# Performance work log

Hardware: AMD Instinct MI355X
Metric: run time of the kernel (lower is better)

Reference implementation:

```python
import jax, jax.numpy as jnp
import numpy as np

B, T, C, H = 4, 2048, 1024, 16
D = C // H

def setup_inputs() -> dict:
    key = jax.random.key(0)
    k1, k2, k3, k4 = jax.random.split(key, 4)
    s = 1.0 / np.sqrt(C)
    return {
        "x": jax.random.normal(k1, (B, T, C), dtype=jnp.float32),
        "W_qkv": jax.random.normal(k2, (3 * C, C), dtype=jnp.float32) * s,
        "W_out": jax.random.normal(k3, (C, C), dtype=jnp.float32) * s,
        "b_out": jax.random.normal(k4, (C,), dtype=jnp.float32) * s,
    }

def reference(x, W_qkv, W_out, b_out):
    Bx, Tx, Cx = x.shape
    # qkv projection (torch Linear: y = x @ W.T), bias=False
    qkv = x @ W_qkv.T                               # [B,T,3C]
    q, k, v = jnp.split(qkv, 3, axis=-1)
    def heads(t):
        return t.reshape(Bx, Tx, H, D).transpose(0, 2, 1, 3)  # [B,H,T,D]
    q, k, v = heads(q), heads(k), heads(v)
    scale = 1.0 / jnp.sqrt(jnp.asarray(D, dtype=x.dtype))
    scores = jnp.einsum("bhqd,bhkd->bhqk", q, k) * scale      # [B,H,T,T]
    causal = jnp.tril(jnp.ones((Tx, Tx), dtype=bool))
    scores = jnp.where(causal[None, None], scores, -jnp.inf)
    attn = jax.nn.softmax(scores, axis=-1)                    # dropout p=0 (eval)
    out = jnp.einsum("bhqk,bhkd->bhqd", attn, v)              # [B,H,T,D]
    out = out.transpose(0, 2, 1, 3).reshape(Bx, Tx, Cx)       # [B,T,C]
    return out @ W_out.T + b_out
```

## Files before the change

### kernel.cpp

```cpp
#include <hip/hip_runtime.h>


typedef __attribute__((ext_vector_type(8))) __bf16 bf16x8;
typedef __attribute__((ext_vector_type(4))) float f32x4;
typedef __attribute__((ext_vector_type(16))) float f32x16;

__device__ __forceinline__ unsigned short f2bf(float f) {
  union { float f; unsigned u; } v; v.f = f;
  unsigned r = v.u + 0x7fffu + ((v.u >> 16) & 1u);
  return (unsigned short)(r >> 16);
}

__device__ __forceinline__ unsigned cvtpk(float lo, float hi) {
  unsigned r;
  asm("v_cvt_pk_bf16_f32 %0, %1, %2" : "=v"(r) : "v"(lo), "v"(hi));
  return r;
}

__device__ __forceinline__ void gld16(const void* g, void* l) {
  __builtin_amdgcn_global_load_lds(
      (const __attribute__((address_space(1))) void*)g,
      (__attribute__((address_space(3))) void*)l, 16, 0, 0);
}

__device__ __forceinline__ f32x4 mfma16(bf16x8 a, bf16x8 b, f32x4 c) {
  return __builtin_amdgcn_mfma_f32_16x16x32_bf16(a, b, c, 0, 0, 0);
}
__device__ __forceinline__ f32x16 mfma32(bf16x8 a, bf16x8 b, f32x16 c) {
  return __builtin_amdgcn_mfma_f32_32x32x16_bf16(a, b, c, 0, 0, 0);
}

__global__ __launch_bounds__(256) void cast_f32_bf16(
    const float* __restrict__ src, unsigned short* __restrict__ dst, int n) {
  int i = (blockIdx.x * 256 + threadIdx.x) * 4;
  if (i >= n) return;
  float4 v = *(const float4*)(src + i);
  ushort4 o;
  o.x = f2bf(v.x); o.y = f2bf(v.y); o.z = f2bf(v.z); o.w = f2bf(v.w);
  *(ushort4*)(dst + i) = o;
}

__device__ __forceinline__ bf16x8 ldsw128(const char* mat, int row, int cb) {
  return *(const bf16x8*)(mat + row * 128 + (cb ^ ((row & 7) << 4)));
}


#define PH_SYNC_A() do { __builtin_amdgcn_s_barrier();              \
    asm volatile("s_waitcnt lgkmcnt(0)" ::: "memory");              \
    __builtin_amdgcn_sched_barrier(0); } while (0)
#define PH_SYNC_B() do { __builtin_amdgcn_s_barrier();              \
    __builtin_amdgcn_sched_barrier(0); } while (0)
#define VMC6() asm volatile("s_waitcnt vmcnt(6)" ::: "memory")
#define VMC0() asm volatile("s_waitcnt vmcnt(0)" ::: "memory")

#define QUAD(MH, NH, AF, BF) do {                                   \
    __builtin_amdgcn_s_setprio(1);                                  \
    _Pragma("unroll") for (int mt = 0; mt < 4; ++mt)                \
    _Pragma("unroll") for (int nt = 0; nt < 2; ++nt)                \
    _Pragma("unroll") for (int kk = 0; kk < 2; ++kk)                \
      acc[(MH)*4+mt][(NH)*2+nt] =                                   \
          mfma16(AF[mt][kk], BF[nt][kk], acc[(MH)*4+mt][(NH)*2+nt]);\
    __builtin_amdgcn_s_setprio(0);                                  \
  } while (0)

__device__ __forceinline__ void stage_half(const char* gbase, char* mat,
                                           int kt, int half, int tid) {
#pragma unroll
  for (int q = 0; q < 2; ++q) {
    const int r = half * 128 + q * 64 + (tid >> 3);
    const int cb = (tid & 7) * 16;
    gld16(gbase + (size_t)r * 2048 + kt * 128 + (cb ^ ((r & 7) << 4)),
          mat + r * 128 + cb);
  }
}

__device__ __forceinline__ void rdA(bf16x8 aF[4][2], const char* mat,
                                    int wm, int mh, int lr, int lg) {
#pragma unroll
  for (int mt = 0; mt < 4; ++mt) {
    const int row = mh * 128 + wm * 64 + mt * 16 + lr;
#pragma unroll
    for (int kk = 0; kk < 2; ++kk)
      aF[mt][kk] = ldsw128(mat, row, kk * 64 + lg * 16);
  }
}
__device__ __forceinline__ void rdB(bf16x8 bF[2][2], const char* mat,
                                    int wn, int nh, int lr, int lg) {
#pragma unroll
  for (int nt = 0; nt < 2; ++nt) {
    const int row = wn * 64 + nh * 32 + nt * 16 + lr;
#pragma unroll
    for (int kk = 0; kk < 2; ++kk)
      bF[nt][kk] = ldsw128(mat, row, kk * 64 + lg * 16);
  }
}

template <int MODE>
__global__ __launch_bounds__(512, 2) void gemm8p(
    const unsigned short* __restrict__ A, const unsigned short* __restrict__ Bm,
    unsigned short* __restrict__ qo, unsigned short* __restrict__ ko,
    unsigned short* __restrict__ vo,
    const float* __restrict__ bias, float* __restrict__ fout) {
  __shared__ char lds[131072];
  const int tid = threadIdx.x;
  const int w = tid >> 6, l = tid & 63, lr = l & 15, lg = l >> 4;
  const int wm = w >> 2, wn = w & 3;
  constexpr int GX = (MODE == 0) ? 12 : 4;
  constexpr int NWG = GX * 32;
  const int L = blockIdx.x + blockIdx.y * GX;
  const int logical = (L & 7) * (NWG >> 3) + (L >> 3);
  const int m0 = (logical / GX) * 256, n0 = (logical % GX) * 256;
  const char* Ag = (const char*)A + (size_t)m0 * 2048;
  const char* Bg = (const char*)Bm + (size_t)n0 * 2048;
  char* A0 = lds;           char* B0 = lds + 32768;
  char* A1 = lds + 65536;   char* B1 = lds + 98304;

  f32x4 acc[8][4];
  f32x4 zero = {0.f, 0.f, 0.f, 0.f};
#pragma unroll
  for (int i = 0; i < 8; i++)
#pragma unroll
    for (int jj = 0; jj < 4; jj++) acc[i][jj] = zero;

  stage_half(Ag, A0, 0, 0, tid);
  stage_half(Ag, A0, 0, 1, tid);
  stage_half(Bg, B0, 0, 0, tid);
  stage_half(Bg, B0, 0, 1, tid);
  stage_half(Ag, A1, 1, 0, tid);
  stage_half(Bg, B1, 1, 0, tid);
  stage_half(Bg, B1, 1, 1, tid);
  VMC6();
  __builtin_amdgcn_s_barrier();
  __builtin_amdgcn_sched_barrier(0);

  for (int j = 0; j < 8; ++j) {
    const int t0 = 2 * j, t1 = 2 * j + 1;
    const bool more = (j < 7);
    bf16x8 aF[4][2], b0F[2][2], b1F[2][2];

    rdA(aF, A0, wm, 0, lr, lg);
    rdB(b0F, B0, wn, 0, lr, lg);
    stage_half(Ag, A1, t1, 1, tid);
    PH_SYNC_A();
    QUAD(0, 0, aF, b0F);
    PH_SYNC_B();
    rdB(b1F, B0, wn, 1, lr, lg);
    if (more) stage_half(Ag, A0, t0 + 2, 0, tid);
    PH_SYNC_A();
    QUAD(0, 1, aF, b1F);
    PH_SYNC_B();
    rdA(aF, A0, wm, 1, lr, lg);
    if (more) stage_half(Bg, B0, t0 + 2, 0, tid);
    PH_SYNC_A();
    QUAD(1, 1, aF, b1F);
    PH_SYNC_B();
    if (more) stage_half(Bg, B0, t0 + 2, 1, tid);
    PH_SYNC_A();
    QUAD(1, 0, aF, b0F);
    if (more) VMC6(); else VMC0();
    PH_SYNC_B();
    rdA(aF, A1, wm, 0, lr, lg);
    rdB(b0F, B1, wn, 0, lr, lg);
    if (more) stage_half(Ag, A0, t0 + 2, 1, tid);
    PH_SYNC_A();
    QUAD(0, 0, aF, b0F);
    PH_SYNC_B();
    rdB(b1F, B1, wn, 1, lr, lg);
    if (more) stage_half(Ag, A1, t1 + 2, 0, tid);
    PH_SYNC_A();
    QUAD(0, 1, aF, b1F);
    PH_SYNC_B();
    rdA(aF, A1, wm, 1, lr, lg);
    if (more) stage_half(Bg, B1, t1 + 2, 0, tid);
    PH_SYNC_A();
    QUAD(1, 1, aF, b1F);
    PH_SYNC_B();
    if (more) stage_half(Bg, B1, t1 + 2, 1, tid);
    PH_SYNC_A();
    QUAD(1, 0, aF, b0F);
    if (more) VMC6();
    PH_SYNC_B();
  }

#pragma unroll
  for (int mt8 = 0; mt8 < 8; ++mt8) {
    const int mh = mt8 >> 2, mt = mt8 & 3;
#pragma unroll
    for (int nt4 = 0; nt4 < 4; ++nt4) {
      int n = n0 + wn * 64 + nt4 * 16 + lr;
      int mbase = m0 + mh * 128 + wm * 64 + mt * 16 + lg * 4;
      if (MODE == 0) {
        int ty = n >> 10, cc = n & 1023;
        int h = cc >> 6, dd = cc & 63;
        unsigned short* dst = (ty == 0) ? qo : ((ty == 1) ? ko : vo);
        float sc = (ty == 0) ? 0.18033688011111687f : 1.0f;
#pragma unroll
        for (int i = 0; i < 4; i++) {
          int m = mbase + i;
          int b = m >> 11, tt = m & 2047;
          dst[(((size_t)(b * 16 + h)) * 2048 + tt) * 64 + dd] =
              f2bf(acc[mt8][nt4][i] * sc);
        }
      } else {
        float bv = bias[n];
#pragma unroll
        for (int i = 0; i < 4; i++) {
          int m = mbase + i;
          fout[(size_t)m * 1024 + n] = acc[mt8][nt4][i] + bv;
        }
      }
    }
  }
}

__global__ __launch_bounds__(256) void transpose_v64(
    const unsigned short* __restrict__ v, unsigned short* __restrict__ vt) {
  __shared__ unsigned short tile[64 * 72];
  int bh = blockIdx.y, t0 = blockIdx.x * 64;
  const unsigned short* vp = v + (size_t)bh * 2048 * 64;
  unsigned short* vtp = vt + (size_t)bh * 64 * 2048;
  int tid = threadIdx.x;
#pragma unroll
  for (int it = 0; it < 2; ++it) {
    int s = tid + it * 256;
    int r = s >> 3, c = (s & 7) * 8;
    *(uint4*)(tile + r * 72 + c) = *(const uint4*)(vp + (size_t)(t0 + r) * 64 + c);
  }
  __syncthreads();
#pragma unroll
  for (int it = 0; it < 2; ++it) {
    int s = tid + it * 256;
    int d = s >> 3, c = (s & 7) * 8;
    unsigned short tmp[8];
#pragma unroll
    for (int j = 0; j < 8; j++) tmp[j] = tile[(c + j) * 72 + d];
    *(uint4*)(vtp + (size_t)d * 2048 + t0 + c) = *(uint4*)tmp;
  }
}

__device__ __forceinline__ bf16x8 ldsw(const char* base, int row, int cb) {
  return *(const bf16x8*)(base + row * 128 + (cb ^ ((row & 7) << 4)));
}

__global__ __launch_bounds__(512, 4) void attn_causal(
    const unsigned short* __restrict__ qg, const unsigned short* __restrict__ kg,
    const unsigned short* __restrict__ vtg, unsigned short* __restrict__ og) {
  __shared__ char lds[32768];
  const int tid = threadIdx.x;
  const int w = tid >> 6, l = tid & 63, lo = l & 31, hi = l >> 5;
  const int bh = blockIdx.x;
  const int qc = (0x31204657u >> (blockIdx.y * 4)) & 7;
  const int q0 = qc * 256;
  const int nkv = qc * 4 + 4;
  const int b = bh >> 4, h = bh & 15;
  const char* kpB = (const char*)(kg + (size_t)bh * 131072);
  const char* vpB = (const char*)(vtg + (size_t)bh * 131072);
  const unsigned short* qp = qg + (size_t)bh * 131072;
  const int qrow = q0 + 8 * lo + w;

  bf16x8 qf[4];
#pragma unroll
  for (int c = 0; c < 4; ++c)
    qf[c] = *(const bf16x8*)(qp + (size_t)qrow * 64 + hi * 8 + c * 16);

  f32x16 ov[2];
#pragma unroll
  for (int r = 0; r < 16; ++r) { ov[0][r] = 0.f; ov[1][r] = 0.f; }
  const f32x16 zz = {0.f, 0.f, 0.f, 0.f, 0.f, 0.f, 0.f, 0.f,
                     0.f, 0.f, 0.f, 0.f, 0.f, 0.f, 0.f, 0.f};
  float m = -__builtin_inff(), lsum = 0.f;

  const int srow = tid >> 3;
  const int scb = ((tid & 7) * 16) ^ ((srow & 7) << 4);

  gld16(kpB + (size_t)srow * 128 + scb, lds + tid * 16);
  gld16(vpB + (size_t)srow * 4096 + scb, lds + 8192 + tid * 16);
  __syncthreads();

  for (int kt = 0; kt < nkv; ++kt) {
    const int k0 = kt * 64;
    if (kt + 1 < nkv) {
      char* nb = lds + ((kt + 1) & 1) * 16384;
      gld16(kpB + (size_t)(k0 + 64 + srow) * 128 + scb, nb + tid * 16);
      gld16(vpB + (size_t)srow * 4096 + (size_t)(k0 + 64) * 2 + scb, nb + 8192 + tid * 16);
    }
    const char* Kbuf = lds + (kt & 1) * 16384;
    const char* Vbuf = Kbuf + 8192;

    f32x16 sv[2];
    __builtin_amdgcn_s_setprio(1);
#pragma unroll
    for (int c = 0; c < 4; ++c) {
      bf16x8 kf0 = ldsw(Kbuf, lo, hi * 16 + c * 32);
      bf16x8 kf1 = ldsw(Kbuf, 32 + lo, hi * 16 + c * 32);
      if (c == 0) {
        sv[0] = mfma32(kf0, qf[0], zz);
        sv[1] = mfma32(kf1, qf[0], zz);
      } else {
        sv[0] = mfma32(kf0, qf[c], sv[0]);
        sv[1] = mfma32(kf1, qf[c], sv[1]);
      }
    }
    __builtin_amdgcn_s_setprio(0);

    if (kt >= nkv - 4) {
#pragma unroll
      for (int t = 0; t < 2; ++t)
#pragma unroll
        for (int r = 0; r < 16; ++r) {
          int kgl = k0 + t * 32 + (r & 3) + 8 * (r >> 2) + 4 * hi;
          if (kgl > qrow) sv[t][r] = -__builtin_inff();
        }
    }

    float mx[16];
#pragma unroll
    for (int i = 0; i < 16; ++i) mx[i] = fmaxf(sv[0][i], sv[1][i]);
#pragma unroll
    for (int s = 8; s > 0; s >>= 1)
#pragma unroll
      for (int i = 0; i < s; ++i) mx[i] = fmaxf(mx[i], mx[i + s]);
    float tm = fmaxf(mx[0], __shfl_xor(mx[0], 32, 64));

    if (!__all(tm <= m + 8.f)) {
      float nm = fmaxf(fmaxf(m, tm), -1e30f);
      float f = exp2f(m - nm);
      m = nm;
      lsum *= f;
#pragma unroll
      for (int r = 0; r < 16; ++r) { ov[0][r] *= f; ov[1][r] *= f; }
    }

    float ps = 0.f;
#pragma unroll
    for (int t = 0; t < 2; ++t)
#pragma unroll
      for (int r = 0; r < 16; ++r) {
        float p = exp2f(sv[t][r] - m);
        sv[t][r] = p;
        ps += p;
      }
    lsum += ps;

    __builtin_amdgcn_s_setprio(1);
#pragma unroll
    for (int c = 0; c < 4; ++c) {
      const int t = c >> 1, rb = (c & 1) * 8;
      unsigned wA = cvtpk(sv[t][rb + 0], sv[t][rb + 1]);
      unsigned wB = cvtpk(sv[t][rb + 2], sv[t][rb + 3]);
      unsigned wC = cvtpk(sv[t][rb + 4], sv[t][rb + 5]);
      unsigned wD = cvtpk(sv[t][rb + 6], sv[t][rb + 7]);
      asm volatile("v_permlane32_swap_b32 %0, %1" : "+v"(wA), "+v"(wC));
      asm volatile("v_permlane32_swap_b32 %0, %1" : "+v"(wB), "+v"(wD));
      union { uint4 u; bf16x8 h; } pc;
      pc.u.x = wA; pc.u.y = wB; pc.u.z = wC; pc.u.w = wD;
      bf16x8 vf0 = ldsw(Vbuf, lo, hi * 16 + c * 32);
      bf16x8 vf1 = ldsw(Vbuf, 32 + lo, hi * 16 + c * 32);
      ov[0] = mfma32(vf0, pc.h, ov[0]);
      ov[1] = mfma32(vf1, pc.h, ov[1]);
    }
    __builtin_amdgcn_s_setprio(0);
    __syncthreads();
  }

  float lt = lsum + __shfl_xor(lsum, 32, 64);
  float inv = 1.0f / lt;
  char* outl = lds + w * 4096;
#pragma unroll
  for (int t2 = 0; t2 < 2; ++t2)
#pragma unroll
    for (int rp = 0; rp < 8; ++rp) {
      const int r = rp * 2;
      const int d0 = (r & 3) + 8 * (r >> 2) + 4 * hi + 32 * t2;
      unsigned pw = cvtpk(ov[t2][r] * inv, ov[t2][r + 1] * inv);
      *(unsigned*)(outl + lo * 128 + ((d0 * 2) ^ ((lo & 7) << 4))) = pw;
    }
  __syncthreads();
  {
    const int qi = l >> 1, cbb = (l & 1) * 64;
    const int t = q0 + 8 * qi + w;
    unsigned short* gp = og + ((size_t)(b * 2048 + t)) * 1024 + h * 64 + (cbb >> 1);
#pragma unroll
    for (int i = 0; i < 4; ++i) {
      uint4 vdat = *(const uint4*)(outl + qi * 128 + ((cbb + i * 16) ^ ((qi & 7) << 4)));
      *(uint4*)(gp + i * 8) = vdat;
    }
  }
}

extern "C" void kernel_launch(void* const* d_in, const int* in_sizes, int n_in,
                              void* d_out, int out_size, void* d_ws, size_t ws_size,
                              hipStream_t stream) {
  const float* x = (const float*)d_in[0];
  const float* Wqkv = (const float*)d_in[1];
  const float* Wout = (const float*)d_in[2];
  const float* bout = (const float*)d_in[3];
  float* out = (float*)d_out;
  char* ws = (char*)d_ws;

  unsigned short* xb = (unsigned short*)(ws);
  unsigned short* wqb = (unsigned short*)(ws + 16777216);
  unsigned short* wob = (unsigned short*)(ws + 23068672);
  unsigned short* qb = (unsigned short*)(ws + 25165824);
  unsigned short* kb = (unsigned short*)(ws + 41943040);
  unsigned short* vb = (unsigned short*)(ws + 58720256);
  unsigned short* vtb = xb;
  unsigned short* ogb = vb;

  cast_f32_bf16<<<8192, 256, 0, stream>>>(x, xb, 8388608);
  cast_f32_bf16<<<3072, 256, 0, stream>>>(Wqkv, wqb, 3145728);
  cast_f32_bf16<<<1024, 256, 0, stream>>>(Wout, wob, 1048576);

  gemm8p<0><<<dim3(12, 32), 512, 0, stream>>>(xb, wqb, qb, kb, vb, nullptr, nullptr);
  transpose_v64<<<dim3(32, 64), 256, 0, stream>>>(vb, vtb);
  attn_causal<<<dim3(64, 8), 512, 0, stream>>>(qb, kb, vtb, ogb);
  gemm8p<1><<<dim3(4, 32), 512, 0, stream>>>(ogb, wob, nullptr, nullptr, nullptr, bout, out);
}
```

Before: 182.2 us.

## Process two query-row sets per wave in causal attention with half the threads

After: 190.9 us. +4.8%, slower.

```diff
diff --git a/kernel.cpp b/kernel.cpp
--- a/kernel.cpp
+++ b/kernel.cpp
@@ -43,7 +43,6 @@
 __device__ __forceinline__ bf16x8 ldsw128(const char* mat, int row, int cb) {
   return *(const bf16x8*)(mat + row * 128 + (cb ^ ((row & 7) << 4)));
 }
-
 
 #define PH_SYNC_A() do { __builtin_amdgcn_s_barrier();              \
     asm volatile("s_waitcnt lgkmcnt(0)" ::: "memory");              \
@@ -242,7 +241,7 @@
   return *(const bf16x8*)(base + row * 128 + (cb ^ ((row & 7) << 4)));
 }
 
-__global__ __launch_bounds__(512, 4) void attn_causal(
+__global__ __launch_bounds__(256, 2) void attn_causal(
     const unsigned short* __restrict__ qg, const unsigned short* __restrict__ kg,
     const unsigned short* __restrict__ vtg, unsigned short* __restrict__ og) {
   __shared__ char lds[32768];
@@ -256,49 +255,68 @@
   const char* kpB = (const char*)(kg + (size_t)bh * 131072);
   const char* vpB = (const char*)(vtg + (size_t)bh * 131072);
   const unsigned short* qp = qg + (size_t)bh * 131072;
-  const int qrow = q0 + 8 * lo + w;
-
-  bf16x8 qf[4];
-#pragma unroll
-  for (int c = 0; c < 4; ++c)
-    qf[c] = *(const bf16x8*)(qp + (size_t)qrow * 64 + hi * 8 + c * 16);
-
-  f32x16 ov[2];
-#pragma unroll
-  for (int r = 0; r < 16; ++r) { ov[0][r] = 0.f; ov[1][r] = 0.f; }
+  const int qrow0 = q0 + 8 * lo + 2 * w;
+  const int qrow1 = qrow0 + 1;
+
+  bf16x8 qf0[4], qf1[4];
+#pragma unroll
+  for (int c = 0; c < 4; ++c) {
+    qf0[c] = *(const bf16x8*)(qp + (size_t)qrow0 * 64 + hi * 8 + c * 16);
+    qf1[c] = *(const bf16x8*)(qp + (size_t)qrow1 * 64 + hi * 8 + c * 16);
+  }
+
+  f32x16 ov0[2], ov1[2];
+#pragma unroll
+  for (int r = 0; r < 16; ++r) {
+    ov0[0][r] = 0.f; ov0[1][r] = 0.f; ov1[0][r] = 0.f; ov1[1][r] = 0.f;
+  }
   const f32x16 zz = {0.f, 0.f, 0.f, 0.f, 0.f, 0.f, 0.f, 0.f,
                      0.f, 0.f, 0.f, 0.f, 0.f, 0.f, 0.f, 0.f};
-  float m = -__builtin_inff(), lsum = 0.f;
+  float m0s = -__builtin_inff(), ls0 = 0.f;
+  float m1s = -__builtin_inff(), ls1 = 0.f;
 
   const int srow = tid >> 3;
-  const int scb = ((tid & 7) * 16) ^ ((srow & 7) << 4);
-
-  gld16(kpB + (size_t)srow * 128 + scb, lds + tid * 16);
-  gld16(vpB + (size_t)srow * 4096 + scb, lds + 8192 + tid * 16);
+  const int scw = ((tid & 7) * 16) ^ ((srow & 7) << 4);
+
+  {
+    char* nb = lds;
+    gld16(kpB + (size_t)srow * 128 + scw, nb + tid * 16);
+    gld16(kpB + (size_t)(srow + 32) * 128 + scw, nb + 4096 + tid * 16);
+    gld16(vpB + (size_t)srow * 4096 + scw, nb + 8192 + tid * 16);
+    gld16(vpB + (size_t)(srow + 32) * 4096 + scw, nb + 12288 + tid * 16);
+  }
   __syncthreads();
 
   for (int kt = 0; kt < nkv; ++kt) {
     const int k0 = kt * 64;
     if (kt + 1 < nkv) {
       char* nb = lds + ((kt + 1) & 1) * 16384;
-      gld16(kpB + (size_t)(k0 + 64 + srow) * 128 + scb, nb + tid * 16);
-      gld16(vpB + (size_t)srow * 4096 + (size_t)(k0 + 64) * 2 + scb, nb + 8192 + tid * 16);
+      const char* ks = kpB + (size_t)(k0 + 64) * 128;
+      const char* vs = vpB + (size_t)(k0 + 64) * 2;
+      gld16(ks + (size_t)srow * 128 + scw, nb + tid * 16);
+      gld16(ks + (size_t)(srow + 32) * 128 + scw, nb + 4096 + tid * 16);
+      gld16(vs + (size_t)srow * 4096 + scw, nb + 8192 + tid * 16);
+      gld16(vs + (size_t)(srow + 32) * 4096 + scw, nb + 12288 + tid * 16);
     }
     const char* Kbuf = lds + (kt & 1) * 16384;
     const char* Vbuf = Kbuf + 8192;
 
-    f32x16 sv[2];
+    f32x16 sv0[2], sv1[2];
     __builtin_amdgcn_s_setprio(1);
 #pragma unroll
     for (int c = 0; c < 4; ++c) {
       bf16x8 kf0 = ldsw(Kbuf, lo, hi * 16 + c * 32);
       bf16x8 kf1 = ldsw(Kbuf, 32 + lo, hi * 16 + c * 32);
       if (c == 0) {
-        sv[0] = mfma32(kf0, qf[0], zz);
-        sv[1] = mfma32(kf1, qf[0], zz);
+        sv0[0] = mfma32(kf0, qf0[0], zz);
+        sv0[1] = mfma32(kf1, qf0[0], zz);
+        sv1[0] = mfma32(kf0, qf1[0], zz);
+        sv1[1] = mfma32(kf1, qf1[0], zz);
       } else {
-        sv[0] = mfma32(kf0, qf[c], sv[0]);
-        sv[1] = mfma32(kf1, qf[c], sv[1]);
+        sv0[0] = mfma32(kf0, qf0[c], sv0[0]);
+        sv0[1] = mfma32(kf1, qf0[c], sv0[1]);
+        sv1[0] = mfma32(kf0, qf1[c], sv1[0]);
+        sv1[1] = mfma32(kf1, qf1[c], sv1[1]);
       }
     }
     __builtin_amdgcn_s_setprio(0);
@@ -309,42 +327,43 @@
 #pragma unroll
         for (int r = 0; r < 16; ++r) {
           int kgl = k0 + t * 32 + (r & 3) + 8 * (r >> 2) + 4 * hi;
-          if (kgl > qrow) sv[t][r] = -__builtin_inff();
+          if (kgl > qrow0) sv0[t][r] = -__builtin_inff();
+          if (kgl > qrow1) sv1[t][r] = -__builtin_inff();
         }
     }
 
-    float mx[16];
-#pragma unroll
-    for (int i = 0; i < 16; ++i) mx[i] = fmaxf(sv[0][i], sv[1][i]);
-#pragma unroll
-    for (int s = 8; s > 0; s >>= 1)
-#pragma unroll
-      for (int i = 0; i < s; ++i) mx[i] = fmaxf(mx[i], mx[i + s]);
-    float tm = fmaxf(mx[0], __shfl_xor(mx[0], 32, 64));
-
-    if (!__all(tm <= m + 8.f)) {
-      float nm = fmaxf(fmaxf(m, tm), -1e30f);
-      float f = exp2f(m - nm);
-      m = nm;
-      lsum *= f;
-#pragma unroll
-      for (int r = 0; r < 16; ++r) { ov[0][r] *= f; ov[1][r] *= f; }
-    }
-
-    float ps = 0.f;
-#pragma unroll
-    for (int t = 0; t < 2; ++t)
-#pragma unroll
-      for (int r = 0; r < 16; ++r) {
-        float p = exp2f(sv[t][r] - m);
-        sv[t][r] = p;
-        ps += p;
+    auto softmax_set = [&](f32x16 (&sv)[2], f32x16 (&ov)[2], float& mm, float& ls) {
+      float mx[16];
+#pragma unroll
+      for (int i = 0; i < 16; ++i) mx[i] = fmaxf(sv[0][i], sv[1][i]);
+#pragma unroll
+      for (int s = 8; s > 0; s >>= 1)
+#pragma unroll
+        for (int i = 0; i < s; ++i) mx[i] = fmaxf(mx[i], mx[i + s]);
+      float tm = fmaxf(mx[0], __shfl_xor(mx[0], 32, 64));
+      if (!__all(tm <= mm + 8.f)) {
+        float nm = fmaxf(fmaxf(mm, tm), -1e30f);
+        float f = exp2f(mm - nm);
+        mm = nm;
+        ls *= f;
+#pragma unroll
+        for (int r = 0; r < 16; ++r) { ov[0][r] *= f; ov[1][r] *= f; }
       }
-    lsum += ps;
-
-    __builtin_amdgcn_s_setprio(1);
-#pragma unroll
-    for (int c = 0; c < 4; ++c) {
+      float ps = 0.f;
+#pragma unroll
+      for (int t = 0; t < 2; ++t)
+#pragma unroll
+        for (int r = 0; r < 16; ++r) {
+          float p = exp2f(sv[t][r] - mm);
+          sv[t][r] = p;
+          ps += p;
+        }
+      ls += ps;
+    };
+    softmax_set(sv0, ov0, m0s, ls0);
+    softmax_set(sv1, ov1, m1s, ls1);
+
+    auto mkpc = [&](f32x16 (&sv)[2], int c) -> bf16x8 {
       const int t = c >> 1, rb = (c & 1) * 8;
       unsigned wA = cvtpk(sv[t][rb + 0], sv[t][rb + 1]);
       unsigned wB = cvtpk(sv[t][rb + 2], sv[t][rb + 3]);
@@ -354,35 +373,48 @@
       asm volatile("v_permlane32_swap_b32 %0, %1" : "+v"(wB), "+v"(wD));
       union { uint4 u; bf16x8 h; } pc;
       pc.u.x = wA; pc.u.y = wB; pc.u.z = wC; pc.u.w = wD;
+      return pc.h;
+    };
+    __builtin_amdgcn_s_setprio(1);
+#pragma unroll
+    for (int c = 0; c < 4; ++c) {
       bf16x8 vf0 = ldsw(Vbuf, lo, hi * 16 + c * 32);
       bf16x8 vf1 = ldsw(Vbuf, 32 + lo, hi * 16 + c * 32);
-      ov[0] = mfma32(vf0, pc.h, ov[0]);
-      ov[1] = mfma32(vf1, pc.h, ov[1]);
+      bf16x8 p0 = mkpc(sv0, c);
+      ov0[0] = mfma32(vf0, p0, ov0[0]);
+      ov0[1] = mfma32(vf1, p0, ov0[1]);
+      bf16x8 p1 = mkpc(sv1, c);
+      ov1[0] = mfma32(vf0, p1, ov1[0]);
+      ov1[1] = mfma32(vf1, p1, ov1[1]);
     }
     __builtin_amdgcn_s_setprio(0);
     __syncthreads();
   }
 
-  float lt = lsum + __shfl_xor(lsum, 32, 64);
-  float inv = 1.0f / lt;
-  char* outl = lds + w * 4096;
+  float lt0 = ls0 + __shfl_xor(ls0, 32, 64);
+  float lt1 = ls1 + __shfl_xor(ls1, 32, 64);
+  float inv0 = 1.0f / lt0, inv1 = 1.0f / lt1;
+  char* outl = lds + w * 8192;
 #pragma unroll
   for (int t2 = 0; t2 < 2; ++t2)
 #pragma unroll
     for (int rp = 0; rp < 8; ++rp) {
       const int r = rp * 2;
       const int d0 = (r & 3) + 8 * (r >> 2) + 4 * hi + 32 * t2;
-      unsigned pw = cvtpk(ov[t2][r] * inv, ov[t2][r + 1] * inv);
-      *(unsigned*)(outl + lo * 128 + ((d0 * 2) ^ ((lo & 7) << 4))) = pw;
+      const int boff = lo * 128 + ((d0 * 2) ^ ((lo & 7) << 4));
+      *(unsigned*)(outl + boff) = cvtpk(ov0[t2][r] * inv0, ov0[t2][r + 1] * inv0);
+      *(unsigned*)(outl + 4096 + boff) = cvtpk(ov1[t2][r] * inv1, ov1[t2][r + 1] * inv1);
     }
   __syncthreads();
-  {
+#pragma unroll
+  for (int s = 0; s < 2; ++s) {
     const int qi = l >> 1, cbb = (l & 1) * 64;
-    const int t = q0 + 8 * qi + w;
+    const int t = q0 + 8 * qi + 2 * w + s;
     unsigned short* gp = og + ((size_t)(b * 2048 + t)) * 1024 + h * 64 + (cbb >> 1);
 #pragma unroll
     for (int i = 0; i < 4; ++i) {
-      uint4 vdat = *(const uint4*)(outl + qi * 128 + ((cbb + i * 16) ^ ((qi & 7) << 4)));
+      uint4 vdat = *(const uint4*)(outl + s * 4096 + qi * 128 +
+                                   ((cbb + i * 16) ^ ((qi & 7) << 4)));
       *(uint4*)(gp + i * 8) = vdat;
     }
   }
@@ -413,6 +445,6 @@
 
   gemm8p<0><<<dim3(12, 32), 512, 0, stream>>>(xb, wqb, qb, kb, vb, nullptr, nullptr);
   transpose_v64<<<dim3(32, 64), 256, 0, stream>>>(vb, vtb);
-  attn_causal<<<dim3(64, 8), 512, 0, stream>>>(qb, kb, vtb, ogb);
+  attn_causal<<<dim3(64, 8), 256, 0, stream>>>(qb, kb, vtb, ogb);
   gemm8p<1><<<dim3(4, 32), 512, 0, stream>>>(ogb, wob, nullptr, nullptr, nullptr, bout, out);
 }
```
